# Kernel optimization log

Measured on AMD Instinct MI355X. Metric: run time of the kernel, lower is better.

## Reference

```python
import jax, jax.numpy as jnp
import numpy as np

MARGIN = 0.5
SCALE = 64.0
EPS = 1e-12  # matches torch F.normalize default eps


def setup_inputs() -> dict:
    key = jax.random.key(0)
    k1, k2, k3 = jax.random.split(key, 3)
    B, D, C = 1024, 512, 100000
    features = jax.random.normal(k1, (B, D), dtype=jnp.float32)
    labels = jax.random.randint(k2, (B,), 0, C, dtype=jnp.int64)
    # xavier_uniform for [C, D] weight: bound = sqrt(6/(C+D))
    bound = np.sqrt(6.0 / (C + D)).astype(np.float32)
    weight = jax.random.uniform(k3, (C, D), dtype=jnp.float32, minval=-bound, maxval=bound)
    return {"features": features, "labels": labels, "weight": weight}


def _l2norm(x):
    # F.normalize(dim=1): x / max(||x||, eps)
    n = jnp.sqrt(jnp.sum(x * x, axis=1, keepdims=True))
    return x / jnp.maximum(n, EPS)


def reference(features, labels, weight):
    f = _l2norm(features)              # [B, D]
    w = _l2norm(weight)                # [C, D]
    cos_theta = f @ w.T                # [B, C]
    B = features.shape[0]
    rows = jnp.arange(B)
    # subtract margin at the label position only (no one-hot materialization)
    cos_m = cos_theta.at[rows, labels].add(-MARGIN)
    logits = cos_m * SCALE
    logZ = jax.nn.logsumexp(logits, axis=1)        # [B]
    tgt = logits[rows, labels]                     # [B]
    loss = jnp.mean(logZ - tgt)
    return loss
```

## Files before the change

kernel.cpp:

```cpp
#include <hip/hip_runtime.h>
#include <hip/hip_bf16.h>
#include <hip/hip_fp8.h>
#include <stdint.h>

#define B_ROWS 1024
#define DIM    512
#define C_CLS  100000
#define C_PAD  100352
#define NT     784
#define NT_PER_XCD 98
#define MT     8
#define NPAD   (C_PAD - C_CLS)

using f32x4 = __attribute__((ext_vector_type(4))) float;
using i32x4 = __attribute__((ext_vector_type(4))) int;
using i32x8 = __attribute__((ext_vector_type(8))) int;

#define AS1(p) ((const __attribute__((address_space(1))) uint32_t*)(p))
#define AS3(p) ((__attribute__((address_space(3))) uint32_t*)(p))
#define SBAR()   __builtin_amdgcn_s_barrier()
#define SCHED0() __builtin_amdgcn_sched_barrier(0)
#define LGKM0()  asm volatile("s_waitcnt lgkmcnt(0)" ::: "memory")
#define VMCNT0() asm volatile("s_waitcnt vmcnt(0)" ::: "memory")

static __device__ __forceinline__ uint32_t f2fp8(float f) {
    __hip_fp8_e4m3 q(f);
    return (uint32_t)q.__x;
}
static __device__ __forceinline__ float fp82f(uint32_t b) {
    __hip_fp8_e4m3 h;
    h.__x = (__hip_fp8_storage_t)b;
    return (float)h;
}

__global__ __launch_bounds__(256) void normalize_rows(
    const float* __restrict__ src, uint8_t* __restrict__ dst, int nvalid, int ntotal)
{
    const int row  = blockIdx.x * 4 + (threadIdx.x >> 6);
    const int lane = threadIdx.x & 63;
    if (row >= ntotal) return;
    uint2* d2 = reinterpret_cast<uint2*>(dst + (size_t)row * DIM);
    if (row >= nvalid) { d2[lane] = make_uint2(0u, 0u); return; }
    const float4* s4 = reinterpret_cast<const float4*>(src + (size_t)row * DIM);
    const float4 a = s4[lane * 2], b = s4[lane * 2 + 1];
    float ss = a.x*a.x + a.y*a.y + a.z*a.z + a.w*a.w
             + b.x*b.x + b.y*b.y + b.z*b.z + b.w*b.w;
    #pragma unroll
    for (int k = 1; k < 64; k <<= 1) ss += __shfl_xor(ss, k);
    const float inv = 1.0f / fmaxf(sqrtf(ss), 1e-12f);
    uint2 o;
    o.x = f2fp8(a.x*inv) | (f2fp8(a.y*inv) << 8) | (f2fp8(a.z*inv) << 16) | (f2fp8(a.w*inv) << 24);
    o.y = f2fp8(b.x*inv) | (f2fp8(b.y*inv) << 8) | (f2fp8(b.z*inv) << 16) | (f2fp8(b.w*inv) << 24);
    d2[lane] = o;
}

__global__ __launch_bounds__(256, 3) void gemm_lse(
    const uint8_t* __restrict__ A,
    const uint8_t* __restrict__ W,
    float* __restrict__ ps)
{
    __shared__ __align__(16) uint8_t lds[2][128 * 128];

    const int tid  = threadIdx.x;
    const int lane = tid & 63;
    const int wid  = tid >> 6;
    const int wm   = wid >> 1;
    const int wn   = wid & 1;

    const int b     = blockIdx.x;
    const int xcd   = b & 7;
    const int j     = b >> 3;
    const int ntile = xcd * NT_PER_XCD + (j >> 3);
    const int mtile = j & 7;

    const uint8_t* Abase = A + (size_t)mtile * 128 * DIM;
    const uint8_t* Bbase = W + (size_t)ntile * 128 * DIM;

    auto stage = [&](int kt) {
        #pragma unroll
        for (int p = 0; p < 4; ++p) {
            const int u   = tid + p * 256;
            const int row = u >> 3;
            const int sub = (u & 7) ^ (row & 7);
            const uint8_t* As = Abase + (size_t)row * DIM + kt * 128 + sub * 16;
            const uint8_t* Bs = Bbase + (size_t)row * DIM + kt * 128 + sub * 16;
            __builtin_amdgcn_global_load_lds(AS1(As), AS3(&lds[0][u * 16]), 16, 0, 0);
            __builtin_amdgcn_global_load_lds(AS1(Bs), AS3(&lds[1][u * 16]), 16, 0, 0);
        }
    };

    const int l15 = lane & 15;
    const int uhi = lane >> 4;

    i32x8 aF[4], bF[4];
    f32x4 acc[4][4] = {};

    auto ldfrag = [&](const uint8_t* base, int row) -> i32x8 {
        const int swz = row & 7;
        const i32x4 lo = *reinterpret_cast<const i32x4*>(base + row * 128 + (((uhi << 1) | 0) ^ swz) * 16);
        const i32x4 hi = *reinterpret_cast<const i32x4*>(base + row * 128 + (((uhi << 1) | 1) ^ swz) * 16);
        i32x8 r;
        r[0] = lo[0]; r[1] = lo[1]; r[2] = lo[2]; r[3] = lo[3];
        r[4] = hi[0]; r[5] = hi[1]; r[6] = hi[2]; r[7] = hi[3];
        return r;
    };

    stage(0);

    #pragma unroll 1
    for (int kt = 0; kt < 4; ++kt) {
        VMCNT0(); SBAR();
        #pragma unroll
        for (int mi = 0; mi < 4; ++mi) aF[mi] = ldfrag(&lds[0][0], wm * 64 + mi * 16 + l15);
        #pragma unroll
        for (int ni = 0; ni < 4; ++ni) bF[ni] = ldfrag(&lds[1][0], wn * 64 + ni * 16 + l15);
        LGKM0(); SCHED0(); SBAR();
        if (kt < 3) stage(kt + 1);
        #pragma unroll
        for (int mi = 0; mi < 4; ++mi)
            #pragma unroll
            for (int ni = 0; ni < 4; ++ni)
                acc[mi][ni] = __builtin_amdgcn_mfma_scale_f32_16x16x128_f8f6f4(
                    aF[mi], bF[ni], acc[mi][ni], 0, 0, 0, 127, 0, 127);
    }

    __syncthreads();
    float* red = reinterpret_cast<float*>(&lds[0][0]);
    #pragma unroll
    for (int mi = 0; mi < 4; ++mi) {
        #pragma unroll
        for (int r = 0; r < 4; ++r) {
            float s = __expf(fmaf(acc[mi][0][r], 64.0f, -64.0f))
                    + __expf(fmaf(acc[mi][1][r], 64.0f, -64.0f))
                    + __expf(fmaf(acc[mi][2][r], 64.0f, -64.0f))
                    + __expf(fmaf(acc[mi][3][r], 64.0f, -64.0f));
            #pragma unroll
            for (int k = 1; k < 16; k <<= 1) s += __shfl_xor(s, k);
            if (l15 == 0) red[(wm * 64 + mi * 16 + uhi * 4 + r) * 2 + wn] = s;
        }
    }
    __syncthreads();
    if (tid < 128)
        ps[(size_t)ntile * B_ROWS + mtile * 128 + tid] = red[tid * 2] + red[tid * 2 + 1];
}

__global__ __launch_bounds__(256) void finalize(
    const float* __restrict__ ps,
    const uint8_t* __restrict__ fb, const uint8_t* __restrict__ wb,
    const int* __restrict__ labels, float* __restrict__ row_loss)
{
    const int row = blockIdx.x;
    const int t   = threadIdx.x;
    const int lab = labels[row];

    const uint8_t* frow = fb + (size_t)row * DIM;
    const uint8_t* wrow = wb + (size_t)lab * DIM;
    uint32_t fa = *reinterpret_cast<const uint16_t*>(frow + 2 * t);
    uint32_t wa = *reinterpret_cast<const uint16_t*>(wrow + 2 * t);
    float d = fp82f(fa & 0xffu) * fp82f(wa & 0xffu)
            + fp82f(fa >> 8)    * fp82f(wa >> 8);
    #pragma unroll
    for (int k = 1; k < 64; k <<= 1) d += __shfl_xor(d, k);

    float s = 0.0f;
    for (int i = t; i < NT; i += 256) s += ps[(size_t)i * B_ROWS + row];
    #pragma unroll
    for (int k = 1; k < 64; k <<= 1) s += __shfl_xor(s, k);

    __shared__ float sd[4], ssm[4];
    if ((t & 63) == 0) { sd[t >> 6] = d; ssm[t >> 6] = s; }
    __syncthreads();
    if (t == 0) {
        const float dt = sd[0] + sd[1] + sd[2] + sd[3];
        float S = ssm[0] + ssm[1] + ssm[2] + ssm[3];
        const float lt = 64.0f * dt;
        S += expf(lt - 96.0f) - expf(lt - 64.0f) - (float)NPAD * expf(-64.0f);
        row_loss[row] = 64.0f + logf(S) - (lt - 32.0f);
    }
}

__global__ __launch_bounds__(256) void mean_k(const float* __restrict__ rl, float* __restrict__ out)
{
    const int t = threadIdx.x;
    float s = 0.0f;
    for (int i = t; i < B_ROWS; i += 256) s += rl[i];
    #pragma unroll
    for (int k = 1; k < 64; k <<= 1) s += __shfl_xor(s, k);
    __shared__ float r4[4];
    if ((t & 63) == 0) r4[t >> 6] = s;
    __syncthreads();
    if (t == 0) out[0] = (r4[0] + r4[1] + r4[2] + r4[3]) * (1.0f / B_ROWS);
}

extern "C" void kernel_launch(void* const* d_in, const int* in_sizes, int n_in,
                              void* d_out, int out_size, void* d_ws, size_t ws_size,
                              hipStream_t stream)
{
    const float* features = (const float*)d_in[0];
    const int*   labels   = (const int*)d_in[1];
    const float* weight   = (const float*)d_in[2];

    char* ws = (char*)d_ws;
    uint8_t* wb = (uint8_t*)ws;
    uint8_t* fb = (uint8_t*)(ws + (size_t)C_PAD * DIM);
    float*   psum = (float*)(ws + (size_t)C_PAD * DIM + (size_t)B_ROWS * DIM);
    float*   rl = psum + (size_t)NT * B_ROWS;

    normalize_rows<<<C_PAD / 4, 256, 0, stream>>>(weight, wb, C_CLS, C_PAD);
    normalize_rows<<<B_ROWS / 4, 256, 0, stream>>>(features, fb, B_ROWS, B_ROWS);
    gemm_lse<<<NT * MT, 256, 0, stream>>>(fb, wb, psum);
    finalize<<<B_ROWS, 256, 0, stream>>>(psum, fb, wb, labels, rl);
    mean_k<<<1, 256, 0, stream>>>(rl, (float*)d_out);
}
```

Baseline: 129.7 us.

## Fuse weight normalization and fp8 quantization into GEMM, keeping the full W tile in LDS

Removes the separate weight-normalize kernel and its fp8 workspace. Each GEMM block now loads its 128 fp32 weight rows, normalizes and quantizes them into a 64KB LDS tile, then loops over all 8 M-tiles of the feature matrix while reusing that tile. The label cosine in finalize is recomputed from the fp32 inputs. This avoids writing and rereading the quantized weight matrix, at the cost of lower occupancy, a serial prologue per block, and fewer, larger blocks.

```diff
diff --git a/kernel.cpp b/kernel.cpp
--- a/kernel.cpp
+++ b/kernel.cpp
@@ -9,7 +9,6 @@
 #define C_PAD  100352
 #define NT     784
 #define NT_PER_XCD 98
-#define MT     8
 #define NPAD   (C_PAD - C_CLS)
 
 using f32x4 = __attribute__((ext_vector_type(4))) float;
@@ -27,20 +26,13 @@
     __hip_fp8_e4m3 q(f);
     return (uint32_t)q.__x;
 }
-static __device__ __forceinline__ float fp82f(uint32_t b) {
-    __hip_fp8_e4m3 h;
-    h.__x = (__hip_fp8_storage_t)b;
-    return (float)h;
-}
 
 __global__ __launch_bounds__(256) void normalize_rows(
-    const float* __restrict__ src, uint8_t* __restrict__ dst, int nvalid, int ntotal)
+    const float* __restrict__ src, uint8_t* __restrict__ dst)
 {
     const int row  = blockIdx.x * 4 + (threadIdx.x >> 6);
     const int lane = threadIdx.x & 63;
-    if (row >= ntotal) return;
     uint2* d2 = reinterpret_cast<uint2*>(dst + (size_t)row * DIM);
-    if (row >= nvalid) { d2[lane] = make_uint2(0u, 0u); return; }
     const float4* s4 = reinterpret_cast<const float4*>(src + (size_t)row * DIM);
     const float4 a = s4[lane * 2], b = s4[lane * 2 + 1];
     float ss = a.x*a.x + a.y*a.y + a.z*a.z + a.w*a.w
@@ -54,12 +46,13 @@
     d2[lane] = o;
 }
 
-__global__ __launch_bounds__(256, 3) void gemm_lse(
+__global__ __launch_bounds__(256, 2) void gemm_fused(
     const uint8_t* __restrict__ A,
-    const uint8_t* __restrict__ W,
+    const float*   __restrict__ Wsrc,
     float* __restrict__ ps)
 {
-    __shared__ __align__(16) uint8_t lds[2][128 * 128];
+    __shared__ __align__(16) uint8_t ldsW[128 * 512];
+    __shared__ __align__(16) uint8_t ldsA[128 * 128];
 
     const int tid  = threadIdx.x;
     const int lane = tid & 63;
@@ -68,112 +61,159 @@
     const int wn   = wid & 1;
 
     const int b     = blockIdx.x;
-    const int xcd   = b & 7;
-    const int j     = b >> 3;
-    const int ntile = xcd * NT_PER_XCD + (j >> 3);
-    const int mtile = j & 7;
-
-    const uint8_t* Abase = A + (size_t)mtile * 128 * DIM;
-    const uint8_t* Bbase = W + (size_t)ntile * 128 * DIM;
-
-    auto stage = [&](int kt) {
+    const int ntile = (b & 7) * NT_PER_XCD + (b >> 3);
+
+    {
+        const int kt_w  = lane >> 4;
+        const int unit  = (lane & 15) >> 1;
+        const int half8 = (lane & 1) * 8;
+        #pragma unroll 1
+        for (int g = 0; g < 32; g += 8) {
+            float4 va[8], vb[8];
+            #pragma unroll
+            for (int i = 0; i < 8; ++i) {
+                const int grow = ntile * 128 + wid * 32 + g + i;
+                if (grow < C_CLS) {
+                    const float4* p = reinterpret_cast<const float4*>(Wsrc + (size_t)grow * DIM) + lane * 2;
+                    va[i] = p[0]; vb[i] = p[1];
+                } else {
+                    va[i] = make_float4(0.f, 0.f, 0.f, 0.f);
+                    vb[i] = make_float4(0.f, 0.f, 0.f, 0.f);
+                }
+            }
+            #pragma unroll
+            for (int i = 0; i < 8; ++i) {
+                const int r = wid * 32 + g + i;
+                float ss = va[i].x*va[i].x + va[i].y*va[i].y + va[i].z*va[i].z + va[i].w*va[i].w
+                         + vb[i].x*vb[i].x + vb[i].y*vb[i].y + vb[i].z*vb[i].z + vb[i].w*vb[i].w;
+                #pragma unroll
+                for (int k = 1; k < 64; k <<= 1) ss += __shfl_xor(ss, k);
+                const float inv = 1.0f / fmaxf(sqrtf(ss), 1e-12f);
+                uint2 o;
+                o.x = f2fp8(va[i].x*inv) | (f2fp8(va[i].y*inv) << 8)
+                    | (f2fp8(va[i].z*inv) << 16) | (f2fp8(va[i].w*inv) << 24);
+                o.y = f2fp8(vb[i].x*inv) | (f2fp8(vb[i].y*inv) << 8)
+                    | (f2fp8(vb[i].z*inv) << 16) | (f2fp8(vb[i].w*inv) << 24);
+                *reinterpret_cast<uint2*>(
+                    &ldsW[r * 512 + kt_w * 128 + ((unit ^ (r & 7)) << 4) + half8]) = o;
+            }
+        }
+    }
+    __syncthreads();
+
+    auto stageA = [&](int mt, int kt) {
         #pragma unroll
         for (int p = 0; p < 4; ++p) {
             const int u   = tid + p * 256;
             const int row = u >> 3;
             const int sub = (u & 7) ^ (row & 7);
-            const uint8_t* As = Abase + (size_t)row * DIM + kt * 128 + sub * 16;
-            const uint8_t* Bs = Bbase + (size_t)row * DIM + kt * 128 + sub * 16;
-            __builtin_amdgcn_global_load_lds(AS1(As), AS3(&lds[0][u * 16]), 16, 0, 0);
-            __builtin_amdgcn_global_load_lds(AS1(Bs), AS3(&lds[1][u * 16]), 16, 0, 0);
+            const uint8_t* As = A + ((size_t)(mt * 128 + row)) * DIM + kt * 128 + sub * 16;
+            __builtin_amdgcn_global_load_lds(AS1(As), AS3(&ldsA[u * 16]), 16, 0, 0);
         }
     };
 
     const int l15 = lane & 15;
     const int uhi = lane >> 4;
 
-    i32x8 aF[4], bF[4];
-    f32x4 acc[4][4] = {};
-
-    auto ldfrag = [&](const uint8_t* base, int row) -> i32x8 {
+    auto ldAf = [&](int mi) -> i32x8 {
+        const int row = wm * 64 + mi * 16 + l15;
         const int swz = row & 7;
-        const i32x4 lo = *reinterpret_cast<const i32x4*>(base + row * 128 + (((uhi << 1) | 0) ^ swz) * 16);
-        const i32x4 hi = *reinterpret_cast<const i32x4*>(base + row * 128 + (((uhi << 1) | 1) ^ swz) * 16);
-        i32x8 r;
-        r[0] = lo[0]; r[1] = lo[1]; r[2] = lo[2]; r[3] = lo[3];
-        r[4] = hi[0]; r[5] = hi[1]; r[6] = hi[2]; r[7] = hi[3];
+        const i32x4 lo = *reinterpret_cast<const i32x4*>(&ldsA[row * 128 + (((uhi << 1) | 0) ^ swz) * 16]);
+        const i32x4 hi = *reinterpret_cast<const i32x4*>(&ldsA[row * 128 + (((uhi << 1) | 1) ^ swz) * 16]);
+        i32x8 r; r[0]=lo[0]; r[1]=lo[1]; r[2]=lo[2]; r[3]=lo[3];
+                 r[4]=hi[0]; r[5]=hi[1]; r[6]=hi[2]; r[7]=hi[3];
         return r;
     };
-
-    stage(0);
+    auto ldBf = [&](int kt, int ni) -> i32x8 {
+        const int row = wn * 64 + ni * 16 + l15;
+        const int swz = row & 7;
+        const uint8_t* base = &ldsW[row * 512 + kt * 128];
+        const i32x4 lo = *reinterpret_cast<const i32x4*>(base + ((((uhi << 1) | 0) ^ swz) << 4));
+        const i32x4 hi = *reinterpret_cast<const i32x4*>(base + ((((uhi << 1) | 1) ^ swz) << 4));
+        i32x8 r; r[0]=lo[0]; r[1]=lo[1]; r[2]=lo[2]; r[3]=lo[3];
+                 r[4]=hi[0]; r[5]=hi[1]; r[6]=hi[2]; r[7]=hi[3];
+        return r;
+    };
+
+    i32x8 aF[4], bF[4];
+
+    stageA(0, 0);
 
     #pragma unroll 1
-    for (int kt = 0; kt < 4; ++kt) {
-        VMCNT0(); SBAR();
+    for (int mt = 0; mt < 8; ++mt) {
+        f32x4 acc[4][4] = {};
         #pragma unroll
-        for (int mi = 0; mi < 4; ++mi) aF[mi] = ldfrag(&lds[0][0], wm * 64 + mi * 16 + l15);
+        for (int kt = 0; kt < 4; ++kt) {
+            VMCNT0(); SBAR();
+            #pragma unroll
+            for (int mi = 0; mi < 4; ++mi) aF[mi] = ldAf(mi);
+            #pragma unroll
+            for (int ni = 0; ni < 4; ++ni) bF[ni] = ldBf(kt, ni);
+            LGKM0(); SCHED0(); SBAR();
+            if (kt < 3) stageA(mt, kt + 1);
+            #pragma unroll
+            for (int mi = 0; mi < 4; ++mi)
+                #pragma unroll
+                for (int ni = 0; ni < 4; ++ni)
+                    acc[mi][ni] = __builtin_amdgcn_mfma_scale_f32_16x16x128_f8f6f4(
+                        aF[mi], bF[ni], acc[mi][ni], 0, 0, 0, 127, 0, 127);
+        }
+        float* red = reinterpret_cast<float*>(&ldsA[0]);
         #pragma unroll
-        for (int ni = 0; ni < 4; ++ni) bF[ni] = ldfrag(&lds[1][0], wn * 64 + ni * 16 + l15);
-        LGKM0(); SCHED0(); SBAR();
-        if (kt < 3) stage(kt + 1);
-        #pragma unroll
-        for (int mi = 0; mi < 4; ++mi)
-            #pragma unroll
-            for (int ni = 0; ni < 4; ++ni)
-                acc[mi][ni] = __builtin_amdgcn_mfma_scale_f32_16x16x128_f8f6f4(
-                    aF[mi], bF[ni], acc[mi][ni], 0, 0, 0, 127, 0, 127);
-    }
-
-    __syncthreads();
-    float* red = reinterpret_cast<float*>(&lds[0][0]);
-    #pragma unroll
-    for (int mi = 0; mi < 4; ++mi) {
-        #pragma unroll
-        for (int r = 0; r < 4; ++r) {
-            float s = __expf(fmaf(acc[mi][0][r], 64.0f, -64.0f))
-                    + __expf(fmaf(acc[mi][1][r], 64.0f, -64.0f))
-                    + __expf(fmaf(acc[mi][2][r], 64.0f, -64.0f))
-                    + __expf(fmaf(acc[mi][3][r], 64.0f, -64.0f));
-            #pragma unroll
-            for (int k = 1; k < 16; k <<= 1) s += __shfl_xor(s, k);
-            if (l15 == 0) red[(wm * 64 + mi * 16 + uhi * 4 + r) * 2 + wn] = s;
-        }
-    }
-    __syncthreads();
-    if (tid < 128)
-        ps[(size_t)ntile * B_ROWS + mtile * 128 + tid] = red[tid * 2] + red[tid * 2 + 1];
+        for (int mi = 0; mi < 4; ++mi) {
+            #pragma unroll
+            for (int r = 0; r < 4; ++r) {
+                float s = __expf(fmaf(acc[mi][0][r], 64.0f, -64.0f))
+                        + __expf(fmaf(acc[mi][1][r], 64.0f, -64.0f))
+                        + __expf(fmaf(acc[mi][2][r], 64.0f, -64.0f))
+                        + __expf(fmaf(acc[mi][3][r], 64.0f, -64.0f));
+                #pragma unroll
+                for (int k = 1; k < 16; k <<= 1) s += __shfl_xor(s, k);
+                if (l15 == 0) red[(wm * 64 + mi * 16 + uhi * 4 + r) * 2 + wn] = s;
+            }
+        }
+        __syncthreads();
+        if (tid < 128)
+            ps[(size_t)ntile * B_ROWS + mt * 128 + tid] = red[tid * 2] + red[tid * 2 + 1];
+        __syncthreads();
+        if (mt < 7) stageA(mt + 1, 0);
+    }
 }
 
 __global__ __launch_bounds__(256) void finalize(
     const float* __restrict__ ps,
-    const uint8_t* __restrict__ fb, const uint8_t* __restrict__ wb,
+    const float* __restrict__ features, const float* __restrict__ weight,
     const int* __restrict__ labels, float* __restrict__ row_loss)
 {
     const int row = blockIdx.x;
     const int t   = threadIdx.x;
     const int lab = labels[row];
 
-    const uint8_t* frow = fb + (size_t)row * DIM;
-    const uint8_t* wrow = wb + (size_t)lab * DIM;
-    uint32_t fa = *reinterpret_cast<const uint16_t*>(frow + 2 * t);
-    uint32_t wa = *reinterpret_cast<const uint16_t*>(wrow + 2 * t);
-    float d = fp82f(fa & 0xffu) * fp82f(wa & 0xffu)
-            + fp82f(fa >> 8)    * fp82f(wa >> 8);
-    #pragma unroll
-    for (int k = 1; k < 64; k <<= 1) d += __shfl_xor(d, k);
+    const float2 f2 = reinterpret_cast<const float2*>(features + (size_t)row * DIM)[t];
+    const float2 w2 = reinterpret_cast<const float2*>(weight + (size_t)lab * DIM)[t];
+    float d  = f2.x * w2.x + f2.y * w2.y;
+    float nf = f2.x * f2.x + f2.y * f2.y;
+    float nw = w2.x * w2.x + w2.y * w2.y;
+    #pragma unroll
+    for (int k = 1; k < 64; k <<= 1) {
+        d += __shfl_xor(d, k); nf += __shfl_xor(nf, k); nw += __shfl_xor(nw, k);
+    }
 
     float s = 0.0f;
     for (int i = t; i < NT; i += 256) s += ps[(size_t)i * B_ROWS + row];
     #pragma unroll
     for (int k = 1; k < 64; k <<= 1) s += __shfl_xor(s, k);
 
-    __shared__ float sd[4], ssm[4];
-    if ((t & 63) == 0) { sd[t >> 6] = d; ssm[t >> 6] = s; }
+    __shared__ float sd[4], sf[4], sw[4], ssm[4];
+    if ((t & 63) == 0) { sd[t>>6] = d; sf[t>>6] = nf; sw[t>>6] = nw; ssm[t>>6] = s; }
     __syncthreads();
     if (t == 0) {
         const float dt = sd[0] + sd[1] + sd[2] + sd[3];
+        const float nft = sf[0] + sf[1] + sf[2] + sf[3];
+        const float nwt = sw[0] + sw[1] + sw[2] + sw[3];
         float S = ssm[0] + ssm[1] + ssm[2] + ssm[3];
-        const float lt = 64.0f * dt;
+        const float cosv = dt / (fmaxf(sqrtf(nft), 1e-12f) * fmaxf(sqrtf(nwt), 1e-12f));
+        const float lt = 64.0f * cosv;
         S += expf(lt - 96.0f) - expf(lt - 64.0f) - (float)NPAD * expf(-64.0f);
         row_loss[row] = 64.0f + logf(S) - (lt - 32.0f);
     }
@@ -201,14 +241,12 @@
     const float* weight   = (const float*)d_in[2];
 
     char* ws = (char*)d_ws;
-    uint8_t* wb = (uint8_t*)ws;
-    uint8_t* fb = (uint8_t*)(ws + (size_t)C_PAD * DIM);
-    float*   psum = (float*)(ws + (size_t)C_PAD * DIM + (size_t)B_ROWS * DIM);
-    float*   rl = psum + (size_t)NT * B_ROWS;
-
-    normalize_rows<<<C_PAD / 4, 256, 0, stream>>>(weight, wb, C_CLS, C_PAD);
-    normalize_rows<<<B_ROWS / 4, 256, 0, stream>>>(features, fb, B_ROWS, B_ROWS);
-    gemm_lse<<<NT * MT, 256, 0, stream>>>(fb, wb, psum);
-    finalize<<<B_ROWS, 256, 0, stream>>>(psum, fb, wb, labels, rl);
+    uint8_t* fb   = (uint8_t*)ws;
+    float*   psum = (float*)(ws + (size_t)B_ROWS * DIM);
+    float*   rl   = psum + (size_t)NT * B_ROWS;
+
+    normalize_rows<<<B_ROWS / 4, 256, 0, stream>>>(features, fb);
+    gemm_fused<<<NT, 256, 0, stream>>>(fb, weight, psum);
+    finalize<<<B_ROWS, 256, 0, stream>>>(psum, features, weight, labels, rl);
     mean_k<<<1, 256, 0, stream>>>(rl, (float*)d_out);
 }
```

Result: slower. 214.6 us (+65.4%).

## Give each wave private LDS tiles to drop block barriers in GEMM loop

Applied to the files above, without the earlier changes.

Each wave now stages its own 64-row A and 64-row B slices into a private LDS region, so the block-wide s_barrier calls in the K loop are removed and waves synchronize only on their own vmcnt/lgkmcnt. The cost is that A and B tiles are loaded twice per block (each wave pair shares rows), doubling global-to-LDS traffic and LDS footprint from 32KB to 64KB. The launch_bounds occupancy hint of 3 blocks is also dropped, which with the larger LDS may reduce resident blocks per CU.

```diff
diff --git a/kernel.cpp b/kernel.cpp
--- a/kernel.cpp
+++ b/kernel.cpp
@@ -18,7 +18,6 @@
 
 #define AS1(p) ((const __attribute__((address_space(1))) uint32_t*)(p))
 #define AS3(p) ((__attribute__((address_space(3))) uint32_t*)(p))
-#define SBAR()   __builtin_amdgcn_s_barrier()
 #define SCHED0() __builtin_amdgcn_sched_barrier(0)
 #define LGKM0()  asm volatile("s_waitcnt lgkmcnt(0)" ::: "memory")
 #define VMCNT0() asm volatile("s_waitcnt vmcnt(0)" ::: "memory")
@@ -54,12 +53,12 @@
     d2[lane] = o;
 }
 
-__global__ __launch_bounds__(256, 3) void gemm_lse(
+__global__ __launch_bounds__(256) void gemm_lse(
     const uint8_t* __restrict__ A,
     const uint8_t* __restrict__ W,
     float* __restrict__ ps)
 {
-    __shared__ __align__(16) uint8_t lds[2][128 * 128];
+    __shared__ __align__(16) uint8_t lds[4][2][64 * 128];
 
     const int tid  = threadIdx.x;
     const int lane = tid & 63;
@@ -73,19 +72,21 @@
     const int ntile = xcd * NT_PER_XCD + (j >> 3);
     const int mtile = j & 7;
 
-    const uint8_t* Abase = A + (size_t)mtile * 128 * DIM;
-    const uint8_t* Bbase = W + (size_t)ntile * 128 * DIM;
+    const uint8_t* Asrc = A + ((size_t)(mtile * 128 + wm * 64)) * DIM;
+    const uint8_t* Bsrc = W + ((size_t)(ntile * 128 + wn * 64)) * DIM;
 
     auto stage = [&](int kt) {
         #pragma unroll
-        for (int p = 0; p < 4; ++p) {
-            const int u   = tid + p * 256;
+        for (int i = 0; i < 8; ++i) {
+            const int u   = lane + i * 64;
             const int row = u >> 3;
             const int sub = (u & 7) ^ (row & 7);
-            const uint8_t* As = Abase + (size_t)row * DIM + kt * 128 + sub * 16;
-            const uint8_t* Bs = Bbase + (size_t)row * DIM + kt * 128 + sub * 16;
-            __builtin_amdgcn_global_load_lds(AS1(As), AS3(&lds[0][u * 16]), 16, 0, 0);
-            __builtin_amdgcn_global_load_lds(AS1(Bs), AS3(&lds[1][u * 16]), 16, 0, 0);
+            __builtin_amdgcn_global_load_lds(
+                AS1(Asrc + (size_t)row * DIM + kt * 128 + sub * 16),
+                AS3(&lds[wid][0][u * 16]), 16, 0, 0);
+            __builtin_amdgcn_global_load_lds(
+                AS1(Bsrc + (size_t)row * DIM + kt * 128 + sub * 16),
+                AS3(&lds[wid][1][u * 16]), 16, 0, 0);
         }
     };
 
@@ -95,26 +96,26 @@
     i32x8 aF[4], bF[4];
     f32x4 acc[4][4] = {};
 
-    auto ldfrag = [&](const uint8_t* base, int row) -> i32x8 {
-        const int swz = row & 7;
-        const i32x4 lo = *reinterpret_cast<const i32x4*>(base + row * 128 + (((uhi << 1) | 0) ^ swz) * 16);
-        const i32x4 hi = *reinterpret_cast<const i32x4*>(base + row * 128 + (((uhi << 1) | 1) ^ swz) * 16);
-        i32x8 r;
-        r[0] = lo[0]; r[1] = lo[1]; r[2] = lo[2]; r[3] = lo[3];
-        r[4] = hi[0]; r[5] = hi[1]; r[6] = hi[2]; r[7] = hi[3];
-        return r;
+    auto ldfrag = [&](int reg, int r) -> i32x8 {
+        const int swz = r & 7;
+        const uint8_t* base = &lds[wid][reg][0];
+        const i32x4 lo = *reinterpret_cast<const i32x4*>(base + r * 128 + (((uhi << 1) | 0) ^ swz) * 16);
+        const i32x4 hi = *reinterpret_cast<const i32x4*>(base + r * 128 + (((uhi << 1) | 1) ^ swz) * 16);
+        i32x8 v; v[0]=lo[0]; v[1]=lo[1]; v[2]=lo[2]; v[3]=lo[3];
+                 v[4]=hi[0]; v[5]=hi[1]; v[6]=hi[2]; v[7]=hi[3];
+        return v;
     };
 
     stage(0);
 
     #pragma unroll 1
     for (int kt = 0; kt < 4; ++kt) {
-        VMCNT0(); SBAR();
-        #pragma unroll
-        for (int mi = 0; mi < 4; ++mi) aF[mi] = ldfrag(&lds[0][0], wm * 64 + mi * 16 + l15);
-        #pragma unroll
-        for (int ni = 0; ni < 4; ++ni) bF[ni] = ldfrag(&lds[1][0], wn * 64 + ni * 16 + l15);
-        LGKM0(); SCHED0(); SBAR();
+        VMCNT0(); SCHED0();
+        #pragma unroll
+        for (int mi = 0; mi < 4; ++mi) aF[mi] = ldfrag(0, mi * 16 + l15);
+        #pragma unroll
+        for (int ni = 0; ni < 4; ++ni) bF[ni] = ldfrag(1, ni * 16 + l15);
+        LGKM0(); SCHED0();
         if (kt < 3) stage(kt + 1);
         #pragma unroll
         for (int mi = 0; mi < 4; ++mi)
@@ -125,7 +126,7 @@
     }
 
     __syncthreads();
-    float* red = reinterpret_cast<float*>(&lds[0][0]);
+    float* red = reinterpret_cast<float*>(&lds[0][0][0]);
     #pragma unroll
     for (int mi = 0; mi < 4; ++mi) {
         #pragma unroll
```

After: 167.0 us. +28.8%, slower.
